# Optimization experiments

Measured on AMD Instinct MI355X. Metric: run time of the kernel, lower is better.

The kernel has to match this reference:

```python
import jax, jax.numpy as jnp
import numpy as np

IOU_THR = 0.5
NEG_POS = 3
CONF_W = 1.0
LOC_W = 1.0


def setup_inputs() -> dict:
    key = jax.random.key(0)
    ks = jax.random.split(key, 6)
    B, A, G = 16, 65536, 32
    ac = jax.random.uniform(ks[0], (B, A, 2))
    asz = jax.random.uniform(ks[1], (B, A, 2)) * 0.28 + 0.02
    anchors = jnp.concatenate([ac - asz / 2, ac + asz / 2], -1)
    gc = jax.random.uniform(ks[2], (B, G, 2))
    gsz = jax.random.uniform(ks[3], (B, G, 2)) * 0.28 + 0.02
    gt_boxes = jnp.concatenate([gc - gsz / 2, gc + gsz / 2], -1)
    bbox_pred = anchors + 0.05 * jax.random.normal(ks[4], (B, A, 4))
    # probabilities strictly inside (0,1) for BCE
    conf_pred = jax.random.uniform(ks[5], (B, A)) * 0.98 + 0.01
    return {"bbox_pred": bbox_pred, "conf_pred": conf_pred,
            "anchors": anchors, "gt_boxes": gt_boxes}


def _box_iou(a, g):
    # a: [A,4] xyxy, g: [G,4] xyxy -> [A,G]
    lt = jnp.maximum(a[:, None, :2], g[None, :, :2])
    rb = jnp.minimum(a[:, None, 2:], g[None, :, 2:])
    wh = jnp.clip(rb - lt, 0.0)
    inter = wh[..., 0] * wh[..., 1]
    area_a = (a[:, 2] - a[:, 0]) * (a[:, 3] - a[:, 1])
    area_g = (g[:, 2] - g[:, 0]) * (g[:, 3] - g[:, 1])
    return inter / (area_a[:, None] + area_g[None, :] - inter)


def _bce(p, t):
    return -(t * jnp.log(p) + (1.0 - t) * jnp.log1p(-p))


def _smooth_l1(x):
    ax = jnp.abs(x)
    return jnp.where(ax < 1.0, 0.5 * ax * ax, ax - 0.5)


def _per_image(bp, cp, an, gt):
    # bp: [A,4] pred boxes, cp: [A] conf, an: [A,4] anchors, gt: [G,4]
    A = cp.shape[0]
    ious = _box_iou(an, gt)                      # [A,G]
    best_gt_iou = ious.max(1)                    # [A]
    best_gt_idx = ious.argmax(1)                 # [A]
    best_anchor_idx = ious.argmax(0)             # [G] force-match each gt
    mask = (best_gt_iou > IOU_THR).at[best_anchor_idx].set(True)
    num_pos = mask.sum()

    # localization loss (center/size parameterization), summed over positives
    matched = gt[best_gt_idx]                    # [A,4]
    pc = (bp[:, :2] + bp[:, 2:]) / 2
    ps = bp[:, 2:] - bp[:, :2]
    gc = (matched[:, :2] + matched[:, 2:]) / 2
    gs = matched[:, 2:] - matched[:, :2]
    loc = _smooth_l1(jnp.concatenate([pc, ps], 1) - jnp.concatenate([gc, gs], 1)).sum(1)
    loc_loss = jnp.where(mask, loc, 0.0).sum()

    # confidence loss with hard negative mining
    t = mask.astype(cp.dtype)
    bce = _bce(cp, t)
    pos_loss = jnp.where(mask, bce, 0.0).sum()
    neg_bce = jnp.where(mask, 0.0, bce)
    num_neg = jnp.minimum(num_pos * NEG_POS, A - num_pos)
    sorted_neg = -jnp.sort(-neg_bce)             # descending
    neg_loss = jnp.where(jnp.arange(A) < num_neg, sorted_neg, 0.0).sum()
    conf_loss = pos_loss / jnp.maximum(num_pos, 1) + neg_loss / jnp.maximum(num_neg, 1)
    return loc_loss, conf_loss, num_pos


def reference(bbox_pred, conf_pred, anchors, gt_boxes):
    loc, conf, npos = jax.vmap(_per_image)(bbox_pred, conf_pred, anchors, gt_boxes)
    B = bbox_pred.shape[0]
    total_npos = jnp.maximum(npos.sum(), 1)
    total_loc = loc.sum() / total_npos * LOC_W
    total_conf = conf.sum() / B * CONF_W
    return total_loc + total_conf
```

## Files before the change

### kernel.cpp

```cpp
#include <hip/hip_runtime.h>

#define BB 16
#define AA 65536
#define GG 32
#define NB 8192
#define KOFF 59904u
#define MBLK (AA / 256)
#define NSEG 16
#define SEGA (AA / NSEG)

__device__ unsigned char      g_mask[(size_t)BB * AA];
__device__ unsigned char      g_bidx[(size_t)BB * AA];
__device__ unsigned long long g_fpart[(size_t)BB * GG * MBLK];
__device__ unsigned int       g_hpart[(size_t)BB * NSEG * (NB/2)];
__device__ float g_spart[BB * NSEG * 2];
__device__ int   g_npart[BB * NSEG];
__device__ float g_loc[BB], g_pos[BB], g_neg[BB];
__device__ int   g_npos[BB], g_nneg[BB];

__device__ __forceinline__ float iou_f(float ax0, float ay0, float ax1, float ay1,
                                       float gx0, float gy0, float gx1, float gy1) {
    float lx = fmaxf(ax0, gx0), ly = fmaxf(ay0, gy0);
    float rx = fminf(ax1, gx1), ry = fminf(ay1, gy1);
    float w = fmaxf(rx - lx, 0.0f), h = fmaxf(ry - ly, 0.0f);
    float inter = w * h;
    float areaa = (ax1 - ax0) * (ay1 - ay0);
    float areag = (gx1 - gx0) * (gy1 - gy0);
    return inter / (areaa + areag - inter);
}

__device__ __forceinline__ float midval(int bin) {
    return __uint_as_float((((unsigned int)bin + KOFF) << 14) | 8192u);
}

__global__ void k_matchforce(const float4* __restrict__ anchors,
                             const float4* __restrict__ gts) {
    __shared__ float4 sg[GG];
    __shared__ unsigned long long wkey[4][GG];
    const int b = blockIdx.y;
    const int t = threadIdx.x;
    if (t < GG) sg[t] = gts[(size_t)b * GG + t];
    __syncthreads();
    const int a = blockIdx.x * 256 + t;
    const int wave = t >> 6, lane = t & 63;
    const float4 av = anchors[(size_t)b * AA + a];
    float best = -1.0f;
    int bg = 0;
#pragma unroll
    for (int g = 0; g < GG; ++g) {
        const float4 gb = sg[g];
        const float v = iou_f(av.x, av.y, av.z, av.w, gb.x, gb.y, gb.z, gb.w);
        if (v > best) { best = v; bg = g; }
        float m = v;
#pragma unroll
        for (int off = 1; off < 64; off <<= 1) m = fmaxf(m, __shfl_xor(m, off, 64));
        const unsigned long long bal = __ballot(v == m);
        const int first = __ffsll((unsigned long long)bal) - 1;
        if (lane == 0) {
            const unsigned int wa = (unsigned int)(blockIdx.x * 256 + wave * 64 + first);
            wkey[wave][g] = ((unsigned long long)__float_as_uint(m) << 32) |
                            (unsigned long long)(0xFFFFFFFFu - wa);
        }
    }
    g_mask[(size_t)b * AA + a] = (best > 0.5f) ? 1 : 0;
    g_bidx[(size_t)b * AA + a] = (unsigned char)bg;
    __syncthreads();
    if (t < GG) {
        unsigned long long k0 = wkey[0][t];
#pragma unroll
        for (int w = 1; w < 4; ++w) { unsigned long long k1 = wkey[w][t]; if (k1 > k0) k0 = k1; }
        g_fpart[((size_t)b * GG + t) * MBLK + blockIdx.x] = k0;
    }
}

__global__ void k_redforce() {
    const int g = blockIdx.x, b = blockIdx.y, t = threadIdx.x;
    __shared__ unsigned long long red[256];
    red[t] = g_fpart[((size_t)b * GG + g) * MBLK + t];
    __syncthreads();
    for (int w = 128; w > 0; w >>= 1) {
        if (t < w) { if (red[t + w] > red[t]) red[t] = red[t + w]; }
        __syncthreads();
    }
    if (t == 0) {
        const unsigned int a = 0xFFFFFFFFu - (unsigned int)(red[0] & 0xFFFFFFFFull);
        g_mask[(size_t)b * AA + a] = 1;
    }
}

__global__ void k_stats(const float4* __restrict__ bbox,
                        const float* __restrict__ conf,
                        const float4* __restrict__ gts) {
    __shared__ float4 sg[GG];
    __shared__ unsigned int hp[NB / 2];
    __shared__ float rf[256], rf2[256];
    __shared__ unsigned int ru[256];
    const int b = blockIdx.y, seg = blockIdx.x, t = threadIdx.x;
    if (t < GG) sg[t] = gts[(size_t)b * GG + t];
    for (int j = t; j < NB / 2; j += 256) hp[j] = 0u;
    __syncthreads();

    const size_t base = (size_t)b * AA + (size_t)seg * SEGA;
    const float4* c4 = (const float4*)(conf + base);
    const uchar4* m4 = (const uchar4*)(g_mask + base);
    const uchar4* x4 = (const uchar4*)(g_bidx + base);
    const float4* bb4 = bbox + base;

    float pos = 0.0f, loc = 0.0f;
    int np = 0;
#pragma unroll
    for (int j = 0; j < SEGA / 1024; ++j) {
        const int idx = j * 256 + t;
        const float4 p4 = c4[idx];
        const uchar4 mm = m4[idx];
        const uchar4 xx = x4[idx];
        const float pv[4] = {p4.x, p4.y, p4.z, p4.w};
        const unsigned char mv[4] = {mm.x, mm.y, mm.z, mm.w};
        const unsigned char xv[4] = {xx.x, xx.y, xx.z, xx.w};
#pragma unroll
        for (int c = 0; c < 4; ++c) {
            const float p = pv[c];
            if (mv[c]) {
                np += 1;
                pos += -logf(p);
                const float4 bv = bb4[4 * idx + c];
                const float4 gb = sg[xv[c]];
                const float d0 = (bv.x + bv.z) * 0.5f - (gb.x + gb.z) * 0.5f;
                const float d1 = (bv.y + bv.w) * 0.5f - (gb.y + gb.w) * 0.5f;
                const float d2 = (bv.z - bv.x) - (gb.z - gb.x);
                const float d3 = (bv.w - bv.y) - (gb.w - gb.y);
                float ds[4] = {d0, d1, d2, d3};
#pragma unroll
                for (int q = 0; q < 4; ++q) {
                    float ax = fabsf(ds[q]);
                    loc += (ax < 1.0f) ? 0.5f * ax * ax : ax - 0.5f;
                }
            } else {
                const float nb = -log1pf(-p);
                int key = (int)(__float_as_uint(nb) >> 14) - (int)KOFF;
                key = key < 0 ? 0 : (key > NB - 1 ? NB - 1 : key);
                atomicAdd(&hp[key >> 1], 1u << ((key & 1) << 4));
            }
        }
    }
    ru[t] = (unsigned int)np; rf[t] = pos; rf2[t] = loc;
    __syncthreads();
    for (int w = 128; w > 0; w >>= 1) {
        if (t < w) { ru[t] += ru[t + w]; rf[t] += rf[t + w]; rf2[t] += rf2[t + w]; }
        __syncthreads();
    }
    if (t == 0) {
        g_npart[b * NSEG + seg] = (int)ru[0];
        g_spart[(b * NSEG + seg) * 2 + 0] = rf[0];
        g_spart[(b * NSEG + seg) * 2 + 1] = rf2[0];
    }
    unsigned int* outp = g_hpart + ((size_t)b * NSEG + seg) * (NB / 2);
    for (int j = t; j < NB / 2; j += 256) outp[j] = hp[j];
}

__global__ void __launch_bounds__(1024) k_select() {
    __shared__ unsigned int hist[NB];
    __shared__ unsigned int ru[1024];
    __shared__ unsigned int s2[32];
    __shared__ float sh_pos, sh_loc;
    __shared__ int sh_np, sh_k, sh_bsel;
    __shared__ unsigned int sh_take;
    __shared__ float rf[1024];

    const int b = blockIdx.x, t = threadIdx.x;
    for (int w = t; w < NB / 2; w += 1024) {
        unsigned int lo = 0, hi = 0;
#pragma unroll
        for (int s = 0; s < NSEG; ++s) {
            const unsigned int v = g_hpart[((size_t)b * NSEG + s) * (NB / 2) + w];
            lo += v & 0xFFFFu; hi += v >> 16;
        }
        hist[2 * w] = lo; hist[2 * w + 1] = hi;
    }
    if (t == 0) {
        int np = 0; float pos = 0.0f, loc = 0.0f;
        for (int s = 0; s < NSEG; ++s) {
            np += g_npart[b * NSEG + s];
            pos += g_spart[(b * NSEG + s) * 2 + 0];
            loc += g_spart[(b * NSEG + s) * 2 + 1];
        }
        sh_np = np; sh_pos = pos; sh_loc = loc;
    }
    __syncthreads();
    const int np_tot = sh_np;

    unsigned int c = 0;
    const int hi = NB - 1 - t * 8;
#pragma unroll
    for (int j = 0; j < 8; ++j) c += hist[hi - j];
    ru[t] = c;
    __syncthreads();
    if (t < 32) {
        unsigned int x = 0;
#pragma unroll
        for (int j = 0; j < 32; ++j) x += ru[t * 32 + j];
        s2[t] = x;
    }
    __syncthreads();
    if (t == 0) {
        int k = 3 * np_tot;
        const int maxneg = AA - np_tot;
        if (k > maxneg) k = maxneg;
        sh_k = k;
        int bsel = NB;
        unsigned int take = 0;
        if (k > 0) {
            unsigned int cum = 0;
            int u = 0;
            while (u < 31 && cum + s2[u] < (unsigned int)k) { cum += s2[u]; ++u; }
            int cc = u * 32;
            while (cc < 1023 && cum + ru[cc] < (unsigned int)k) { cum += ru[cc]; ++cc; }
            const int h2 = NB - 1 - cc * 8;
            int j = 0;
            while (j < 7 && cum + hist[h2 - j] < (unsigned int)k) { cum += hist[h2 - j]; ++j; }
            bsel = h2 - j;
            take = (unsigned int)k - cum;
        }
        sh_bsel = bsel; sh_take = take;
    }
    __syncthreads();
    const int bsel = sh_bsel;
    float negp = 0.0f;
    for (int j = t; j < NB; j += 1024)
        if (j > bsel) { unsigned int cnt = hist[j]; if (cnt) negp += (float)cnt * midval(j); }
    rf[t] = negp;
    __syncthreads();
    for (int w = 512; w > 0; w >>= 1) {
        if (t < w) rf[t] += rf[t + w];
        __syncthreads();
    }
    if (t == 0) {
        float neg = 0.0f;
        if (sh_k > 0) neg = rf[0] + (float)sh_take * midval(bsel < NB ? bsel : 0);
        g_loc[b] = sh_loc; g_pos[b] = sh_pos; g_neg[b] = neg;
        g_npos[b] = np_tot; g_nneg[b] = sh_k;
    }
}

__global__ void k_final(unsigned int* __restrict__ out) {
    if (threadIdx.x == 0) {
        float loc = 0.0f, conf = 0.0f;
        int tot = 0;
        for (int b = 0; b < BB; ++b) {
            loc += g_loc[b];
            const int np = g_npos[b], nn = g_nneg[b];
            conf += g_pos[b] / (float)(np > 1 ? np : 1) +
                    g_neg[b] / (float)(nn > 1 ? nn : 1);
            tot += np;
        }
        const float total = loc / (float)(tot > 1 ? tot : 1) + conf / (float)BB;
        unsigned int u = __float_as_uint(total);
        unsigned int r = 0x7FFFu + ((u >> 16) & 1u);
        unsigned int bf = (u + r) >> 16;
        out[0] = (bf << 16) | bf;
    }
}

extern "C" void kernel_launch(void* const* d_in, const int* in_sizes, int n_in,
                              void* d_out, int out_size, void* d_ws, size_t ws_size,
                              hipStream_t stream) {
    const float4* bbox    = (const float4*)d_in[0];
    const float*  conf    = (const float*)d_in[1];
    const float4* anchors = (const float4*)d_in[2];
    const float4* gts     = (const float4*)d_in[3];

    k_matchforce<<<dim3(MBLK, BB), 256, 0, stream>>>(anchors, gts);
    k_redforce<<<dim3(GG, BB), 256, 0, stream>>>();
    k_stats<<<dim3(NSEG, BB), 256, 0, stream>>>(bbox, conf, gts);
    k_select<<<BB, 1024, 0, stream>>>();
    k_final<<<1, 64, 0, stream>>>((unsigned int*)d_out);
}
```

Measured before the change: 153.4 us.

## Accumulate per-thread force-match argmax over multiple anchors before wave reduction

Each thread in the match kernel now processes eight anchors and keeps a running best IoU and anchor index per ground-truth box in registers. The 64-bit key wave reduction then runs once per block instead of once per anchor per gt, which cuts the shuffle-heavy inner loop. The partials shrink to 32 per (image, gt), so the force-reduction kernel becomes one block where each thread serially scans 32 partials. The cost is fewer blocks, lower occupancy and higher register pressure from the 64 per-gt registers.

```diff
diff --git a/kernel.cpp b/kernel.cpp
--- a/kernel.cpp
+++ b/kernel.cpp
@@ -5,7 +5,8 @@
 #define GG 32
 #define NB 8192
 #define KOFF 59904u
-#define MBLK (AA / 256)
+#define MBLK 32
+#define APT 8
 #define NSEG 16
 #define SEGA (AA / NSEG)
 
@@ -18,74 +19,82 @@
 __device__ float g_loc[BB], g_pos[BB], g_neg[BB];
 __device__ int   g_npos[BB], g_nneg[BB];
 
-__device__ __forceinline__ float iou_f(float ax0, float ay0, float ax1, float ay1,
-                                       float gx0, float gy0, float gx1, float gy1) {
-    float lx = fmaxf(ax0, gx0), ly = fmaxf(ay0, gy0);
-    float rx = fminf(ax1, gx1), ry = fminf(ay1, gy1);
-    float w = fmaxf(rx - lx, 0.0f), h = fmaxf(ry - ly, 0.0f);
-    float inter = w * h;
-    float areaa = (ax1 - ax0) * (ay1 - ay0);
-    float areag = (gx1 - gx0) * (gy1 - gy0);
-    return inter / (areaa + areag - inter);
-}
-
 __device__ __forceinline__ float midval(int bin) {
     return __uint_as_float((((unsigned int)bin + KOFF) << 14) | 8192u);
 }
 
-__global__ void k_matchforce(const float4* __restrict__ anchors,
-                             const float4* __restrict__ gts) {
-    __shared__ float4 sg[GG];
+__global__ void __launch_bounds__(256) k_matchforce(
+        const float4* __restrict__ anchors, const float4* __restrict__ gts) {
     __shared__ unsigned long long wkey[4][GG];
-    const int b = blockIdx.y;
-    const int t = threadIdx.x;
-    if (t < GG) sg[t] = gts[(size_t)b * GG + t];
-    __syncthreads();
-    const int a = blockIdx.x * 256 + t;
+    const int b = blockIdx.y, t = threadIdx.x;
     const int wave = t >> 6, lane = t & 63;
-    const float4 av = anchors[(size_t)b * AA + a];
-    float best = -1.0f;
-    int bg = 0;
+    const float4* __restrict__ gts4 = gts + (size_t)b * GG;
+    const float4* __restrict__ ap   = anchors + (size_t)b * AA;
+    const int base = blockIdx.x * (256 * APT);
+
+    float        fm[GG];
+    unsigned int fa[GG];
+#pragma unroll
+    for (int g = 0; g < GG; ++g) { fm[g] = -1.0f; fa[g] = 0u; }
+
+#pragma unroll 2
+    for (int j = 0; j < APT; ++j) {
+        const int aidx = base + j * 256 + t;
+        const float4 a4 = ap[aidx];
+        const float areaa = (a4.z - a4.x) * (a4.w - a4.y);
+        float best = -1.0f;
+        int bg = 0;
+#pragma unroll
+        for (int g = 0; g < GG; ++g) {
+            const float4 gb = gts4[g];
+            const float lx = fmaxf(a4.x, gb.x), ly = fmaxf(a4.y, gb.y);
+            const float rx = fminf(a4.z, gb.z), ry = fminf(a4.w, gb.w);
+            const float w = fmaxf(rx - lx, 0.0f), h = fmaxf(ry - ly, 0.0f);
+            const float inter = w * h;
+            const float ag = (gb.z - gb.x) * (gb.w - gb.y);
+            const float v = inter / (areaa + ag - inter);
+            if (v > best) { best = v; bg = g; }
+            if (v > fm[g]) { fm[g] = v; fa[g] = (unsigned int)aidx; }
+        }
+        g_mask[(size_t)b * AA + aidx] = (best > 0.5f) ? 1 : 0;
+        g_bidx[(size_t)b * AA + aidx] = (unsigned char)bg;
+    }
+
 #pragma unroll
     for (int g = 0; g < GG; ++g) {
-        const float4 gb = sg[g];
-        const float v = iou_f(av.x, av.y, av.z, av.w, gb.x, gb.y, gb.z, gb.w);
-        if (v > best) { best = v; bg = g; }
-        float m = v;
-#pragma unroll
-        for (int off = 1; off < 64; off <<= 1) m = fmaxf(m, __shfl_xor(m, off, 64));
-        const unsigned long long bal = __ballot(v == m);
-        const int first = __ffsll((unsigned long long)bal) - 1;
-        if (lane == 0) {
-            const unsigned int wa = (unsigned int)(blockIdx.x * 256 + wave * 64 + first);
-            wkey[wave][g] = ((unsigned long long)__float_as_uint(m) << 32) |
-                            (unsigned long long)(0xFFFFFFFFu - wa);
-        }
-    }
-    g_mask[(size_t)b * AA + a] = (best > 0.5f) ? 1 : 0;
-    g_bidx[(size_t)b * AA + a] = (unsigned char)bg;
+        unsigned long long key =
+            ((unsigned long long)__float_as_uint(fm[g]) << 32) |
+            (unsigned long long)(0xFFFFFFFFu - fa[g]);
+#pragma unroll
+        for (int off = 1; off < 64; off <<= 1) {
+            const unsigned long long o = __shfl_xor(key, off, 64);
+            if (o > key) key = o;
+        }
+        if (lane == 0) wkey[wave][g] = key;
+    }
     __syncthreads();
     if (t < GG) {
         unsigned long long k0 = wkey[0][t];
 #pragma unroll
-        for (int w = 1; w < 4; ++w) { unsigned long long k1 = wkey[w][t]; if (k1 > k0) k0 = k1; }
+        for (int w = 1; w < 4; ++w) {
+            const unsigned long long k1 = wkey[w][t];
+            if (k1 > k0) k0 = k1;
+        }
         g_fpart[((size_t)b * GG + t) * MBLK + blockIdx.x] = k0;
     }
 }
 
 __global__ void k_redforce() {
-    const int g = blockIdx.x, b = blockIdx.y, t = threadIdx.x;
-    __shared__ unsigned long long red[256];
-    red[t] = g_fpart[((size_t)b * GG + g) * MBLK + t];
-    __syncthreads();
-    for (int w = 128; w > 0; w >>= 1) {
-        if (t < w) { if (red[t + w] > red[t]) red[t] = red[t + w]; }
-        __syncthreads();
-    }
-    if (t == 0) {
-        const unsigned int a = 0xFFFFFFFFu - (unsigned int)(red[0] & 0xFFFFFFFFull);
-        g_mask[(size_t)b * AA + a] = 1;
-    }
+    const int i = threadIdx.x;
+    const int b = i >> 5;
+    unsigned long long best = 0ull;
+#pragma unroll 4
+    for (int s = 0; s < MBLK; ++s) {
+        const unsigned long long v = g_fpart[(size_t)i * MBLK + s];
+        if (v > best) best = v;
+    }
+    const unsigned int a = 0xFFFFFFFFu - (unsigned int)(best & 0xFFFFFFFFull);
+    g_mask[(size_t)b * AA + a] = 1;
 }
 
 __global__ void k_stats(const float4* __restrict__ bbox,
@@ -270,7 +279,7 @@
     const float4* gts     = (const float4*)d_in[3];
 
     k_matchforce<<<dim3(MBLK, BB), 256, 0, stream>>>(anchors, gts);
-    k_redforce<<<dim3(GG, BB), 256, 0, stream>>>();
+    k_redforce<<<1, BB * GG, 0, stream>>>();
     k_stats<<<dim3(NSEG, BB), 256, 0, stream>>>(bbox, conf, gts);
     k_select<<<BB, 1024, 0, stream>>>();
     k_final<<<1, 64, 0, stream>>>((unsigned int*)d_out);
```

Result: slower. 166.9 us (+8.8%).
